# Optimization experiments

Measured on AMD Instinct MI355X. Metric: run time of the kernel, lower is better.

The kernel has to match this reference:

```python
import jax, jax.numpy as jnp
import numpy as np

B, S, D, H = 2, 2048, 1024, 16


def setup_inputs() -> dict:
    key = jax.random.key(0)
    kq, kk, kv1, kv2 = jax.random.split(key, 4)
    return {
        "q": jax.random.normal(kq, (B, S, D), dtype=jnp.float32),
        "k": jax.random.normal(kk, (B, S, D), dtype=jnp.float32),
        "v1": jax.random.normal(kv1, (B, S, D), dtype=jnp.float32),
        "v2": jax.random.normal(kv2, (B, S, D), dtype=jnp.float32),
        "num_attn_heads": 16,
    }


def _split_heads(x, h):
    b, s, d = x.shape
    return x.reshape(b, s, h, d // h).transpose(0, 2, 1, 3)  # [B,H,S,dh]


def reference(q, k, v1, v2, num_attn_heads):
    h = num_attn_heads
    b, s, d = q.shape
    dh = d // h
    qh = _split_heads(q, h)
    kh = _split_heads(k, h)
    v1h = _split_heads(v1, h)
    v2h = _split_heads(v2, h)
    scores = jnp.einsum("bhqd,bhkd->bhqk", qh, kh) / jnp.sqrt(jnp.float32(dh))
    # Faithful to create_mask(input, 0): nopeek = triu(ones, k=0); mask = (nopeek == 0)
    # -> only STRICTLY lower triangle is visible; diagonal and above get -1e9.
    # Row 0 is fully masked -> softmax uniform (same as torch behavior).
    allowed = jnp.tril(jnp.ones((s, s), dtype=bool), k=-1)  # [S,S] j < i
    scores = jnp.where(allowed[None, None], scores, jnp.float32(-1e9))
    p_attn = jax.nn.softmax(scores, axis=-1)  # dropout p=0.0 -> identity
    o1 = jnp.einsum("bhqk,bhkd->bhqd", p_attn, v1h)
    o2 = jnp.einsum("bhqk,bhkd->bhqd", p_attn, v2h)
    o1 = o1.transpose(0, 2, 1, 3).reshape(b, s, d)
    o2 = o2.transpose(0, 2, 1, 3).reshape(b, s, d)
    return (o1, o2)
```

## Files before the change

### kernel.cpp

```cpp
#include <hip/hip_runtime.h>

#define B_ 2
#define S_ 2048
#define D_ 1024
#define H_ 16
#define DH 64
#define OFF2 (B_ * S_ * D_)
#define ELEMS (B_ * H_ * S_ * DH)

typedef __attribute__((ext_vector_type(8))) __bf16 bf16x8;
typedef __attribute__((ext_vector_type(4))) float f32x4;
typedef __attribute__((ext_vector_type(4))) unsigned int u32x4;
typedef __attribute__((ext_vector_type(2))) unsigned int u32x2;
typedef __attribute__((address_space(3))) unsigned int lds_u32;
typedef __attribute__((address_space(1))) const unsigned int glob_u32;

__device__ __forceinline__ unsigned short f2bf(float f) {
    return __builtin_bit_cast(unsigned short, (__bf16)f);
}
__device__ __forceinline__ unsigned int pk2(float a, float b) {
    return (unsigned int)f2bf(a) | ((unsigned int)f2bf(b) << 16);
}
__device__ __forceinline__ float bf2f(unsigned short h) {
    unsigned int u = ((unsigned int)h) << 16;
    return __builtin_bit_cast(float, u);
}

__global__ void prep_all(const float* __restrict__ k,
                         const float* __restrict__ v1, const float* __restrict__ v2,
                         unsigned short* __restrict__ kb,
                         unsigned short* __restrict__ v1t, unsigned short* __restrict__ v2t) {
    int id = blockIdx.x;
    if (id < 2048) {
        int cid = id * 256 + threadIdx.x;
        int d8 = cid & 7;
        int s  = (cid >> 3) & (S_ - 1);
        int h  = (cid >> 14) & (H_ - 1);
        int b  = cid >> 18;
        int off = (b * S_ + s) * D_ + h * DH + d8 * 8;
        float4 f0 = *(const float4*)(k + off);
        float4 f1 = *(const float4*)(k + off + 4);
        u32x4 wv = {pk2(f0.x, f0.y), pk2(f0.z, f0.w),
                    pk2(f1.x, f1.y), pk2(f1.z, f1.w)};
        *(u32x4*)(kb + cid * 8) = wv;
        return;
    }
    __shared__ __align__(16) unsigned short ldsT[64][72];
    int id2 = id - 2048;
    int t = threadIdx.x;
    int s0 = (id2 & 31) * 64;
    int bh = (id2 >> 5) & 31;
    int b = bh >> 4, h = bh & 15;
    const float* src = (id2 >> 10) ? v2 : v1;
    unsigned short* dst = (id2 >> 10) ? v2t : v1t;
    {
        int sl = t >> 2, dc = t & 3;
        int off = (b * S_ + s0 + sl) * D_ + h * DH + dc * 16;
#pragma unroll
        for (int i4 = 0; i4 < 4; i4++) {
            float4 f = *(const float4*)(src + off + i4 * 4);
            int d = dc * 16 + i4 * 4;
            ldsT[d + 0][sl] = f2bf(f.x);
            ldsT[d + 1][sl] = f2bf(f.y);
            ldsT[d + 2][sl] = f2bf(f.z);
            ldsT[d + 3][sl] = f2bf(f.w);
        }
    }
    __syncthreads();
    {
        int d = t >> 2, sc = t & 3;
        u32x4 a = *(const u32x4*)(&ldsT[d][sc * 16]);
        u32x4 c = *(const u32x4*)(&ldsT[d][sc * 16 + 8]);
        int off = (bh * DH + d) * S_ + s0 + sc * 16;
        *(u32x4*)(dst + off) = a;
        *(u32x4*)(dst + off + 8) = c;
    }
}

__global__ __launch_bounds__(256) void flash_attn(
        const float* __restrict__ qf, const unsigned short* __restrict__ kb,
        const unsigned short* __restrict__ v1t, const unsigned short* __restrict__ v2t,
        float* __restrict__ out) {
    __shared__ __align__(16) unsigned short sK0[4096], sK1[4096];
    __shared__ __align__(16) unsigned short sV1[4096], sV2[4096];

    int tid = threadIdx.x;
    int id = blockIdx.x;

    if (id >= 1024) {
        int wid = (id - 1024) * 4 + (tid >> 6);
        int lane = tid & 63;
        int tz = wid >> 11;
        int bhd = wid & 2047;
        const unsigned short* src = (tz ? v2t : v1t) + bhd * S_;
        float sum = 0.f;
#pragma unroll
        for (int kk = 0; kk < 4; kk++) {
            u32x4 v = *(const u32x4*)(src + (kk * 64 + lane) * 8);
#pragma unroll
            for (int jj = 0; jj < 4; jj++) {
                unsigned int u = v[jj];
                sum += bf2f((unsigned short)(u & 0xffff)) + bf2f((unsigned short)(u >> 16));
            }
        }
#pragma unroll
        for (int msk = 32; msk >= 1; msk >>= 1) sum += __shfl_xor(sum, msk, 64);
        if (lane == 0) {
            int b = bhd >> 10, rem = bhd & 1023, h = rem >> 6, d = rem & 63;
            out[tz * OFF2 + b * (S_ * D_) + h * DH + d] = sum * (1.0f / S_);
        }
        return;
    }

    int w = tid >> 6, lane = tid & 63;
    int lr = lane & 15, lg = lane >> 4;
    int srow = tid >> 3, sco = tid & 7;

    int xcd = id & 7;
    int j = id >> 3;
    int bh = xcd * 4 + (j & 3);
    int qt = 31 - (j >> 2);
    int b = bh >> 4, hh = bh & 15;

    const unsigned short* gK  = kb  + bh * (S_ * DH);
    const unsigned short* gV1 = v1t + bh * (DH * S_);
    const unsigned short* gV2 = v2t + bh * (DH * S_);

    auto stageV = [&](int t) {
#pragma unroll
        for (int jj = 0; jj < 2; jj++) {
            int row = srow + jj * 32;
            int cosw = (sco ^ (row & 7)) * 8;
            int c8 = (tid + jj * 256) * 8;
            __builtin_amdgcn_global_load_lds((glob_u32*)(gV1 + row * S_ + t * 64 + cosw),
                                             (lds_u32*)(sV1 + c8), 16, 0, 0);
            __builtin_amdgcn_global_load_lds((glob_u32*)(gV2 + row * S_ + t * 64 + cosw),
                                             (lds_u32*)(sV2 + c8), 16, 0, 0);
        }
    };
    auto stageK = [&](unsigned short* dK, int t) {
#pragma unroll
        for (int jj = 0; jj < 2; jj++) {
            int row = srow + jj * 32;
            int cosw = (sco ^ (row & 7)) * 8;
            int c8 = (tid + jj * 256) * 8;
            __builtin_amdgcn_global_load_lds((glob_u32*)(gK + (t * 64 + row) * 64 + cosw),
                                             (lds_u32*)(dK + c8), 16, 0, 0);
        }
    };

    const float* qsrc = qf + ((size_t)b * S_ + qt * 64 + w * 16 + lr) * D_ + hh * DH + lg * 8;
    float4 q0 = *(const float4*)qsrc;
    float4 q1 = *(const float4*)(qsrc + 4);
    float4 q2 = *(const float4*)(qsrc + 32);
    float4 q3 = *(const float4*)(qsrc + 36);

    stageK(sK0, 0);
    stageV(0);
    stageK(sK1, (qt >= 1) ? 1 : 0);

    bf16x8 qa[2];
    {
        const float qs = 0.125f * 1.4426950408889634f;
        u32x4 w0 = {pk2(q0.x * qs, q0.y * qs), pk2(q0.z * qs, q0.w * qs),
                    pk2(q1.x * qs, q1.y * qs), pk2(q1.z * qs, q1.w * qs)};
        u32x4 w1 = {pk2(q2.x * qs, q2.y * qs), pk2(q2.z * qs, q2.w * qs),
                    pk2(q3.x * qs, q3.y * qs), pk2(q3.z * qs, q3.w * qs)};
        qa[0] = __builtin_bit_cast(bf16x8, w0);
        qa[1] = __builtin_bit_cast(bf16x8, w1);
    }

    f32x4 acc1[4], acc2[4];
#pragma unroll
    for (int dt = 0; dt < 4; dt++) {
        acc1[dt] = (f32x4){0.f, 0.f, 0.f, 0.f};
        acc2[dt] = (f32x4){0.f, 0.f, 0.f, 0.f};
    }
    float l = 0.f;

    for (int t = 0; t <= qt; t++) {
        const unsigned short* cK = (t & 1) ? sK1 : sK0;
        unsigned short* nK       = (t & 1) ? sK0 : sK1;
        if (t > 0) {
            __builtin_amdgcn_s_barrier();
            stageV(t);
            stageK(nK, (t < qt) ? t + 1 : qt);
        }
        asm volatile("s_waitcnt vmcnt(6)" ::: "memory");
        f32x4 s[4];
        __builtin_amdgcn_s_setprio(1);
#pragma unroll
        for (int n = 0; n < 4; n++) {
            int kv = n * 16 + lr;
            int ix0 = ((kv << 6) + lg * 8) ^ ((kv & 7) << 3);
            int ix1 = ((kv << 6) + 32 + lg * 8) ^ ((kv & 7) << 3);
            bf16x8 k0 = __builtin_bit_cast(bf16x8, *(const u32x4*)(cK + ix0));
            bf16x8 k1 = __builtin_bit_cast(bf16x8, *(const u32x4*)(cK + ix1));
            f32x4 a = __builtin_amdgcn_mfma_f32_16x16x32_bf16(
                k0, qa[0], (f32x4){-20.f, -20.f, -20.f, -20.f}, 0, 0, 0);
            s[n] = __builtin_amdgcn_mfma_f32_16x16x32_bf16(k1, qa[1], a, 0, 0, 0);
        }
        __builtin_amdgcn_s_setprio(0);
        if (t == qt) {
#pragma unroll
            for (int n = 0; n < 4; n++)
#pragma unroll
                for (int r = 0; r < 4; r++)
                    if (n * 16 + lg * 4 + r >= w * 16 + lr) s[n][r] = -1e30f;
        }
        u32x4 pa[2];
#pragma unroll
        for (int ks = 0; ks < 2; ks++) {
            float p0[4], p1[4];
#pragma unroll
            for (int r = 0; r < 4; r++) {
                p0[r] = __builtin_amdgcn_exp2f(s[2 * ks][r]);
                p1[r] = __builtin_amdgcn_exp2f(s[2 * ks + 1][r]);
                l += p0[r] + p1[r];
            }
            unsigned int u0 = pk2(p0[0], p0[1]);
            unsigned int u1 = pk2(p0[2], p0[3]);
            unsigned int u2 = pk2(p1[0], p1[1]);
            unsigned int u3 = pk2(p1[2], p1[3]);
            u32x2 ab = __builtin_amdgcn_permlane32_swap(u0, u2, false, false);
            u32x2 cd = __builtin_amdgcn_permlane32_swap(u1, u3, false, false);
            u32x2 ab2 = __builtin_amdgcn_permlane16_swap(ab[0], ab[1], false, false);
            u32x2 cd2 = __builtin_amdgcn_permlane16_swap(cd[0], cd[1], false, false);
            pa[ks] = (u32x4){ab2[0], cd2[0], ab2[1], cd2[1]};
        }
        asm volatile("s_waitcnt vmcnt(2)" ::: "memory");
        __builtin_amdgcn_s_barrier();
        __builtin_amdgcn_s_setprio(1);
#pragma unroll
        for (int ks = 0; ks < 2; ks++) {
            bf16x8 pab = __builtin_bit_cast(bf16x8, pa[ks]);
#pragma unroll
            for (int dt = 0; dt < 4; dt++) {
                int d = dt * 16 + lr;
                int vix = ((d << 6) + ks * 32 + lg * 8) ^ ((d & 7) << 3);
                bf16x8 vf1 = __builtin_bit_cast(bf16x8, *(const u32x4*)(sV1 + vix));
                acc1[dt] = __builtin_amdgcn_mfma_f32_16x16x32_bf16(vf1, pab, acc1[dt], 0, 0, 0);
                bf16x8 vf2 = __builtin_bit_cast(bf16x8, *(const u32x4*)(sV2 + vix));
                acc2[dt] = __builtin_amdgcn_mfma_f32_16x16x32_bf16(vf2, pab, acc2[dt], 0, 0, 0);
            }
        }
        __builtin_amdgcn_s_setprio(0);
    }

    asm volatile("s_waitcnt vmcnt(0)" ::: "memory");

    float lt = l;
    lt += __shfl_xor(lt, 16, 64);
    lt += __shfl_xor(lt, 32, 64);
    float inv = 1.0f / lt;
    {
        int qrow = qt * 64 + w * 16 + lr;
        if (qrow != 0) {
            int base = (b * S_ + qrow) * D_ + hh * DH + lg * 4;
#pragma unroll
            for (int dt = 0; dt < 4; dt++) {
                f32x4 o1 = acc1[dt] * inv;
                f32x4 o2 = acc2[dt] * inv;
                *(f32x4*)(out + base + dt * 16) = o1;
                *(f32x4*)(out + base + dt * 16 + OFF2) = o2;
            }
        }
    }
}

extern "C" void kernel_launch(void* const* d_in, const int* in_sizes, int n_in,
                              void* d_out, int out_size, void* d_ws, size_t ws_size,
                              hipStream_t stream) {
    const float* q  = (const float*)d_in[0];
    const float* k  = (const float*)d_in[1];
    const float* v1 = (const float*)d_in[2];
    const float* v2 = (const float*)d_in[3];
    float* out = (float*)d_out;

    unsigned short* kb  = (unsigned short*)d_ws;
    unsigned short* v1t = kb + ELEMS;
    unsigned short* v2t = v1t + ELEMS;

    prep_all<<<4096, 256, 0, stream>>>(k, v1, v2, kb, v1t, v2t);
    flash_attn<<<2048, 256, 0, stream>>>(q, kb, v1t, v2t, out);
}
```

Baseline: 61.95 us.

## Double-buffer V tiles alongside K and prefetch both one tile ahead

Turns the single V1/V2 shared-memory buffers into double buffers indexed by tile parity. Each iteration now prefetches both K and V for the next tile, and the mid-loop vmcnt(2) wait before the PV MFMAs is removed. V load latency can then overlap a full iteration of compute instead of only the QK^T and softmax phase. The cost is more LDS per block (48KB instead of 32KB), which may lower the number of resident blocks per CU.

```diff
diff --git a/kernel.cpp b/kernel.cpp
--- a/kernel.cpp
+++ b/kernel.cpp
@@ -81,8 +81,9 @@
         const float* __restrict__ qf, const unsigned short* __restrict__ kb,
         const unsigned short* __restrict__ v1t, const unsigned short* __restrict__ v2t,
         float* __restrict__ out) {
-    __shared__ __align__(16) unsigned short sK0[4096], sK1[4096];
-    __shared__ __align__(16) unsigned short sV1[4096], sV2[4096];
+    __shared__ __align__(16) unsigned short sK[2][4096];
+    __shared__ __align__(16) unsigned short sV1[2][4096];
+    __shared__ __align__(16) unsigned short sV2[2][4096];
 
     int tid = threadIdx.x;
     int id = blockIdx.x;
@@ -126,26 +127,26 @@
     const unsigned short* gV1 = v1t + bh * (DH * S_);
     const unsigned short* gV2 = v2t + bh * (DH * S_);
 
-    auto stageV = [&](int t) {
+    auto stageK = [&](int t, int buf) {
+#pragma unroll
+        for (int jj = 0; jj < 2; jj++) {
+            int row = srow + jj * 32;
+            int cosw = (sco ^ (row & 7)) * 8;
+            int c8 = (tid + jj * 256) * 8;
+            __builtin_amdgcn_global_load_lds((glob_u32*)(gK + (t * 64 + row) * 64 + cosw),
+                                             (lds_u32*)(sK[buf] + c8), 16, 0, 0);
+        }
+    };
+    auto stageV = [&](int t, int buf) {
 #pragma unroll
         for (int jj = 0; jj < 2; jj++) {
             int row = srow + jj * 32;
             int cosw = (sco ^ (row & 7)) * 8;
             int c8 = (tid + jj * 256) * 8;
             __builtin_amdgcn_global_load_lds((glob_u32*)(gV1 + row * S_ + t * 64 + cosw),
-                                             (lds_u32*)(sV1 + c8), 16, 0, 0);
+                                             (lds_u32*)(sV1[buf] + c8), 16, 0, 0);
             __builtin_amdgcn_global_load_lds((glob_u32*)(gV2 + row * S_ + t * 64 + cosw),
-                                             (lds_u32*)(sV2 + c8), 16, 0, 0);
-        }
-    };
-    auto stageK = [&](unsigned short* dK, int t) {
-#pragma unroll
-        for (int jj = 0; jj < 2; jj++) {
-            int row = srow + jj * 32;
-            int cosw = (sco ^ (row & 7)) * 8;
-            int c8 = (tid + jj * 256) * 8;
-            __builtin_amdgcn_global_load_lds((glob_u32*)(gK + (t * 64 + row) * 64 + cosw),
-                                             (lds_u32*)(dK + c8), 16, 0, 0);
+                                             (lds_u32*)(sV2[buf] + c8), 16, 0, 0);
         }
     };
 
@@ -155,9 +156,13 @@
     float4 q2 = *(const float4*)(qsrc + 32);
     float4 q3 = *(const float4*)(qsrc + 36);
 
-    stageK(sK0, 0);
-    stageV(0);
-    stageK(sK1, (qt >= 1) ? 1 : 0);
+    stageK(0, 0);
+    stageV(0, 0);
+    {
+        int t1 = (qt >= 1) ? 1 : 0;
+        stageK(t1, 1);
+        stageV(t1, 1);
+    }
 
     bf16x8 qa[2];
     {
@@ -179,14 +184,14 @@
     float l = 0.f;
 
     for (int t = 0; t <= qt; t++) {
-        const unsigned short* cK = (t & 1) ? sK1 : sK0;
-        unsigned short* nK       = (t & 1) ? sK0 : sK1;
         if (t > 0) {
             __builtin_amdgcn_s_barrier();
-            stageV(t);
-            stageK(nK, (t < qt) ? t + 1 : qt);
+            int tn = (t < qt) ? t + 1 : qt;
+            stageK(tn, (t + 1) & 1);
+            stageV(tn, (t + 1) & 1);
         }
         asm volatile("s_waitcnt vmcnt(6)" ::: "memory");
+        const unsigned short* cK = sK[t & 1];
         f32x4 s[4];
         __builtin_amdgcn_s_setprio(1);
 #pragma unroll
@@ -228,8 +233,9 @@
             u32x2 cd2 = __builtin_amdgcn_permlane16_swap(cd[0], cd[1], false, false);
             pa[ks] = (u32x4){ab2[0], cd2[0], ab2[1], cd2[1]};
         }
-        asm volatile("s_waitcnt vmcnt(2)" ::: "memory");
         __builtin_amdgcn_s_barrier();
+        const unsigned short* cV1 = sV1[t & 1];
+        const unsigned short* cV2 = sV2[t & 1];
         __builtin_amdgcn_s_setprio(1);
 #pragma unroll
         for (int ks = 0; ks < 2; ks++) {
@@ -238,9 +244,9 @@
             for (int dt = 0; dt < 4; dt++) {
                 int d = dt * 16 + lr;
                 int vix = ((d << 6) + ks * 32 + lg * 8) ^ ((d & 7) << 3);
-                bf16x8 vf1 = __builtin_bit_cast(bf16x8, *(const u32x4*)(sV1 + vix));
+                bf16x8 vf1 = __builtin_bit_cast(bf16x8, *(const u32x4*)(cV1 + vix));
                 acc1[dt] = __builtin_amdgcn_mfma_f32_16x16x32_bf16(vf1, pab, acc1[dt], 0, 0, 0);
-                bf16x8 vf2 = __builtin_bit_cast(bf16x8, *(const u32x4*)(sV2 + vix));
+                bf16x8 vf2 = __builtin_bit_cast(bf16x8, *(const u32x4*)(cV2 + vix));
                 acc2[dt] = __builtin_amdgcn_mfma_f32_16x16x32_bf16(vf2, pab, acc2[dt], 0, 0, 0);
             }
         }
```

Measured after the change: 62.46 us. Within noise of the previous version (+0.8%).
